# Optimization experiments

Measured on AMD Instinct MI355X. Metric: run time of the kernel, lower is better.

## Reference

```python
import jax, jax.numpy as jnp
from jax import lax
import numpy as np

NUM_KIND = 4
V, H, B = 34, 32, 4096   # raw vertical (2 rows dropped), horizontal, batch
KS = 33                  # odd-rounded max(V-2, H)
NUM_DEPTH = 4
N_SQ = 100


def _conv(x, w):
    # x: (N,1,h,w), w: (1,1,KS,KS); torch Conv2d == cross-correlation == lax default
    return lax.conv_general_dilated(x, w, (1, 1), 'SAME',
                                    dimension_numbers=('NCHW', 'OIHW', 'NCHW'))


def _conv_k(x, w):
    # x: (K,B,1,h,w) -> conv each map with the shared 1-channel kernel
    k, b, c, h, wd = x.shape
    return _conv(x.reshape(k * b, c, h, wd), w).reshape(k, b, c, h, wd)


def setup_inputs() -> dict:
    key = jax.random.key(0)
    ks = jax.random.split(key, 8)
    std = 0.3
    return {
        'dots':    jax.random.randint(ks[0], (V, H, B), 0, NUM_KIND + 1, dtype=jnp.int32),
        'w_each':  jax.random.normal(ks[1], (1, 1, KS, KS), jnp.float32) * std,
        'w_not':   jax.random.normal(ks[2], (1, 1, KS, KS), jnp.float32) * std,
        'w_not2':  jax.random.normal(ks[3], (1, 1, KS, KS), jnp.float32) * std,
        'w_empty': jax.random.normal(ks[4], (1, 1, KS, KS), jnp.float32) * std,
        'W1':      jax.random.normal(ks[5], (N_SQ, (V - 2) * H), jnp.float32) * std,
        'W2':      jax.random.normal(ks[6], (N_SQ, N_SQ), jnp.float32) * std,
        'W3':      jax.random.normal(ks[7], (1, N_SQ), jnp.float32) * std,
    }


def reference(dots, w_each, w_not, w_not2, w_empty, W1, W2, W3):
    # drop last 2 vertical rows, layout (V-2,H,B) -> (B,1,V-2,H)
    board = dots[:-2].astype(jnp.float32).transpose(2, 0, 1)[:, None]  # (B,1,h,w)

    empty = (board == 0).astype(jnp.float32)
    E = _conv(empty, w_empty)                                           # (B,1,h,w)

    kinds = jnp.arange(1, NUM_KIND + 1, dtype=board.dtype).reshape(NUM_KIND, 1, 1, 1, 1)
    each = (board[None] == kinds).astype(jnp.float32)                   # (K,B,1,h,w)
    notm = ((each + empty[None]) == 0).astype(jnp.float32)              # (K,B,1,h,w)

    # first pass: per-color value, masked to that color's cells
    notm_conv = _conv_k(notm, w_not)      # note: the torch code LOGS the convolved not-mask
    v = _conv_k(each, w_each) + E[None] - notm_conv
    L = each * v                          # each_color_value_log (masked)
    s = jax.nn.sigmoid(L.sum(axis=0))     # all_color_value_2nd, (B,1,h,w)

    # iterative diffusion; torch mutates the log in-place each depth:
    # L <- mask * (L + E + conv2nd(notm_conv * before)); before is detached
    for _ in range(NUM_DEPTH):
        before = lax.stop_gradient(s)
        C = _conv_k(notm_conv * before[None], w_not2)
        L = each * (L + E[None] + C)
        s = jax.nn.sigmoid(L.sum(axis=0))

    feat = s.reshape(s.shape[0], -1)      # (B, (V-2)*H)
    x = jax.nn.leaky_relu(feat @ W1.T, 0.2)
    x = jax.nn.leaky_relu(x @ W2.T, 0.2)
    return x @ W3.T                        # (B,1)
```

## Files before the change

### kernel.cpp

```cpp
#include <hip/hip_runtime.h>
#include <cstdint>
#include <cstddef>


typedef _Float16 f16;
typedef __attribute__((ext_vector_type(8))) _Float16 f16x8;
typedef __attribute__((ext_vector_type(4))) float f32x4;

#define NB   4096
#define PIX  1024
#define MR   (NB * 4)

__device__ __forceinline__ void gld_lds16(const void* g, void* l) {
    __builtin_amdgcn_global_load_lds(
        (const __attribute__((address_space(1))) void*)g,
        (__attribute__((address_space(3))) void*)l, 16, 0, 0);
}

__global__ void build_all(const float* __restrict__ we, const float* __restrict__ wn,
                          const float* __restrict__ wn2, const float* __restrict__ wem,
                          const float* __restrict__ W1, const int* __restrict__ dots,
                          f16* __restrict__ Me, f16* __restrict__ Mn,
                          f16* __restrict__ Mn2, f16* __restrict__ Mem,
                          f16* __restrict__ W1b, unsigned char* __restrict__ board) {
    __shared__ unsigned char tile[64][68];
    int bi = blockIdx.x, t = threadIdx.x;
    if (bi < 4096) {
        int idx = bi * 256 + t;
        int o = idx >> 10, in = idx & 1023;
        int i = o >> 5, j = o & 31, a = in >> 5, b = in & 31;
        int u = a - i + 16, v = b - j + 16;
        bool ok = (u >= 0) && (u < 33) && (v >= 0) && (v < 33);
        int w = u * 33 + v;
        float ve = 0.f, vn = 0.f, vn2 = 0.f, vem = 0.f;
        if (ok) { ve = we[w]; vn = wn[w]; vn2 = wn2[w]; vem = wem[w]; }
        Me[idx]  = (f16)ve;
        Mn[idx]  = (f16)vn;
        Mn2[idx] = (f16)vn2;
        Mem[idx] = (f16)vem;
    } else if (bi < 4608) {
        int idx = (bi - 4096) * 256 + t;
        int j = idx >> 10, i = idx & 1023;
        W1b[idx] = (f16)(j < 100 ? W1[j * 1024 + i] : 0.f);
    } else {
        int bb = bi - 4608;
        int bp = bb & 15, bn = bb >> 4;
        int p0 = bp * 64, n0 = bn * 64;
        int ln = t & 63, lp = t >> 6;
#pragma unroll
        for (int j = 0; j < 16; j++) {
            int p = lp * 16 + j;
            tile[p][ln] = (unsigned char)dots[(size_t)(p0 + p) * 4096 + n0 + ln];
        }
        __syncthreads();
#pragma unroll
        for (int j = 0; j < 16; j++) {
            int n = lp * 16 + j;
            board[(size_t)(n0 + n) * 1024 + p0 + ln] = tile[ln][n];
        }
    }
}

__global__ void expand_masks(const unsigned char* __restrict__ board,
                             f16* __restrict__ eachF, f16* __restrict__ notmF,
                             f16* __restrict__ emptyF) {
    int bi = blockIdx.x, t = threadIdx.x;
    if (bi < 8192) {
        int idx = bi * 256 + t;
        int r = idx >> 7, w0 = (idx & 127) << 3;
        int n = r >> 2, k1 = (r & 3) + 1;
        uint64_t bb = *(const uint64_t*)(board + (size_t)n * 1024 + w0);
        f16x8 e, m;
#pragma unroll
        for (int j = 0; j < 8; j++) {
            int bj = (int)((bb >> (8 * j)) & 0xff);
            e[j] = (bj == k1) ? (f16)1.f : (f16)0.f;
            m[j] = (bj != 0 && bj != k1) ? (f16)1.f : (f16)0.f;
        }
        *(f16x8*)(eachF + (size_t)idx * 8) = e;
        *(f16x8*)(notmF + (size_t)idx * 8) = m;
    } else {
        int idx = (bi - 8192) * 256 + t;
        int n = idx >> 7, w0 = (idx & 127) << 3;
        uint64_t bb = *(const uint64_t*)(board + (size_t)n * 1024 + w0);
        f16x8 e;
#pragma unroll
        for (int j = 0; j < 8; j++)
            e[j] = (((bb >> (8 * j)) & 0xff) == 0) ? (f16)1.f : (f16)0.f;
        *(f16x8*)(emptyF + (size_t)idx * 8) = e;
    }
}

template <int MODE>
__device__ __forceinline__ void run_gemm(
    int bjob, int ypx, int nx, char* smem,
    const f16* __restrict__ X, const f16* __restrict__ B,
    const unsigned char* __restrict__ board, const f16* __restrict__ En,
    const f16* __restrict__ NCs, f16* __restrict__ Lsel,
    f16* __restrict__ Sout, f16* __restrict__ outB, int ldo) {
    char* smB = smem;
    char* smA = smem + 16384;

    const int tid = threadIdx.x;
    const int wv = tid >> 6, ln = tid & 63;
    const int wm = wv >> 1, wn_ = wv & 1;
    const int lr = ln & 15, lq = ln >> 4;

    int xcd = bjob & 7, slot = bjob >> 3;
    int bx = slot % nx;
    int by = xcd * ypx + slot / nx;
    const int rtile = by * 128, otile = bx * 128;

    const f32x4 fz = {0.f, 0.f, 0.f, 0.f};
    f32x4 acc[4][4];
#pragma unroll
    for (int i = 0; i < 4; i++)
#pragma unroll
        for (int j = 0; j < 4; j++) acc[i][j] = fz;

    for (int kb = 0; kb < 1024; kb += 64) {
#pragma unroll
        for (int t = 0; t < 4; t++) {
            int c = (wv * 4 + t) * 64 + ln;
            int row = c >> 3, gcol = (c & 7) ^ (row & 7);
            gld_lds16(B + (size_t)(otile + row) * 1024 + kb + gcol * 8, smB + c * 16);
            gld_lds16(X + (size_t)(rtile + row) * 1024 + kb + gcol * 8, smA + c * 16);
        }
        __syncthreads();

#pragma unroll
        for (int kk = 0; kk < 2; kk++) {
            const int oct = kk * 4 + lq;
            f16x8 af[4], bfr[4];
#pragma unroll
            for (int i = 0; i < 4; i++) {
                int rrow = wm * 64 + i * 16 + lr;
                af[i] = *(const f16x8*)(smA + rrow * 128 + (oct ^ (rrow & 7)) * 16);
            }
#pragma unroll
            for (int j = 0; j < 4; j++) {
                int brow = wn_ * 64 + j * 16 + lr;
                bfr[j] = *(const f16x8*)(smB + brow * 128 + (oct ^ (brow & 7)) * 16);
            }
#pragma unroll
            for (int i = 0; i < 4; i++)
#pragma unroll
                for (int j = 0; j < 4; j++)
                    acc[i][j] = __builtin_amdgcn_mfma_f32_16x16x32_f16(
                        af[i], bfr[j], acc[i][j], 0, 0, 0);
        }
        __syncthreads();
    }

#pragma unroll
    for (int i = 0; i < 4; i++) {
        int rbase = rtile + wm * 64 + i * 16 + lq * 4;
#pragma unroll
        for (int j = 0; j < 4; j++) {
            int o = otile + wn_ * 64 + j * 16 + lr;
            f32x4 a = acc[i][j];
            if (MODE == 0) {
#pragma unroll
                for (int v = 0; v < 4; v++)
                    outB[(size_t)(rbase + v) * ldo + o] = (f16)a[v];
            } else {
                int n = rbase >> 2;
                size_t no = (size_t)n * PIX + o;
                int c = board[no];
                float L = 0.f;
                if (c > 0) {
                    float asel = (c == 1) ? a[0] : (c == 2) ? a[1]
                               : (c == 3) ? a[2] : a[3];
                    float ncsel = (float)NCs[(size_t)(rbase + c - 1) * PIX + o];
                    L = asel + (float)En[no] - ncsel;
                }
                Lsel[no] = (f16)L;
                Sout[no] = (f16)(1.f / (1.f + __expf(-L)));
            }
        }
    }
}

__global__ void __launch_bounds__(256, 4) gemm_faA(
    const f16* __restrict__ Mn, const f16* __restrict__ Mem,
    const f16* __restrict__ notmF, const f16* __restrict__ emptyF,
    f16* __restrict__ NC, f16* __restrict__ En) {
    __shared__ __attribute__((aligned(16))) char smem[32768];
    int bi = blockIdx.x;
    if (bi < 1024) {
        run_gemm<0>(bi, 16, 8, smem, notmF, Mn, nullptr, nullptr,
                    nullptr, nullptr, nullptr, NC, PIX);
    } else {
        run_gemm<0>(bi - 1024, 4, 8, smem, emptyF, Mem, nullptr, nullptr,
                    nullptr, nullptr, nullptr, En, PIX);
    }
}

__global__ void __launch_bounds__(256, 4) gemm_faB(
    const f16* __restrict__ Me, const f16* __restrict__ eachF,
    const unsigned char* __restrict__ board, const f16* __restrict__ En,
    const f16* __restrict__ NC, f16* __restrict__ Lsel, f16* __restrict__ S1) {
    __shared__ __attribute__((aligned(16))) char smem[32768];
    run_gemm<2>(blockIdx.x, 16, 8, smem, eachF, Me, board, En, NC,
                Lsel, S1, nullptr, 0);
}

__global__ void __launch_bounds__(256, 2) gemm_depth(
    const f16* __restrict__ NC, const f16* __restrict__ Mn2,
    const unsigned char* __restrict__ board, const f16* __restrict__ En,
    const f16* __restrict__ Sin, f16* __restrict__ Lsel,
    f16* __restrict__ Sout) {
    __shared__ __attribute__((aligned(16))) char smem[36864];
    char* smB = smem;
    char* smA = smem + 16384;
    char* smS = smem + 32768;

    const int tid = threadIdx.x;
    const int wv = tid >> 6, ln = tid & 63;
    const int wm = wv >> 1, wn_ = wv & 1;
    const int lr = ln & 15, lq = ln >> 4;

    int bi = blockIdx.x;
    int xcd = bi & 7, slot = bi >> 3;
    int bx = slot & 7;
    int by = xcd * 16 + (slot >> 3);
    const int rtile = by * 128, otile = bx * 128;
    const int n0 = rtile >> 2;

    const f32x4 fz = {0.f, 0.f, 0.f, 0.f};
    f32x4 acc[4][4];
#pragma unroll
    for (int i = 0; i < 4; i++)
#pragma unroll
        for (int j = 0; j < 4; j++) acc[i][j] = fz;

    for (int kb = 0; kb < 1024; kb += 64) {
#pragma unroll
        for (int t = 0; t < 4; t++) {
            int c = (wv * 4 + t) * 64 + ln;
            int row = c >> 3, gcol = (c & 7) ^ (row & 7);
            gld_lds16(Mn2 + (size_t)(otile + row) * 1024 + kb + gcol * 8, smB + c * 16);
            gld_lds16(NC  + (size_t)(rtile + row) * 1024 + kb + gcol * 8, smA + c * 16);
        }
        {
            int row = tid >> 3, col = tid & 7;
            gld_lds16(Sin + (size_t)(n0 + row) * 1024 + kb + col * 8, smS + tid * 16);
        }
        __syncthreads();

#pragma unroll
        for (int kk = 0; kk < 2; kk++) {
            const int oct = kk * 4 + lq;
            f16x8 af[4], bfr[4];
#pragma unroll
            for (int i = 0; i < 4; i++) {
                int rrow = wm * 64 + i * 16 + lr;
                f16x8 nv = *(const f16x8*)(smA + rrow * 128 + (oct ^ (rrow & 7)) * 16);
                f16x8 sv = *(const f16x8*)(smS + (rrow >> 2) * 128 + oct * 16);
                af[i] = nv * sv;
            }
#pragma unroll
            for (int j = 0; j < 4; j++) {
                int brow = wn_ * 64 + j * 16 + lr;
                bfr[j] = *(const f16x8*)(smB + brow * 128 + (oct ^ (brow & 7)) * 16);
            }
#pragma unroll
            for (int i = 0; i < 4; i++)
#pragma unroll
                for (int j = 0; j < 4; j++)
                    acc[i][j] = __builtin_amdgcn_mfma_f32_16x16x32_f16(
                        af[i], bfr[j], acc[i][j], 0, 0, 0);
        }
        __syncthreads();
    }

#pragma unroll
    for (int i = 0; i < 4; i++) {
        int rbase = rtile + wm * 64 + i * 16 + lq * 4;
#pragma unroll
        for (int j = 0; j < 4; j++) {
            int o = otile + wn_ * 64 + j * 16 + lr;
            f32x4 a = acc[i][j];
            int n = rbase >> 2;
            size_t no = (size_t)n * PIX + o;
            int c = board[no];
            float Lnew = 0.f;
            if (c > 0) {
                float asel = (c == 1) ? a[0] : (c == 2) ? a[1]
                           : (c == 3) ? a[2] : a[3];
                Lnew = (float)Lsel[no] + (float)En[no] + asel;
            }
            Lsel[no] = (f16)Lnew;
            Sout[no] = (f16)(1.f / (1.f + __expf(-Lnew)));
        }
    }
}

__global__ void __launch_bounds__(256) gemm_mlp_fused(
    const f16* __restrict__ feat, const f16* __restrict__ W1b,
    const float* __restrict__ W2, const float* __restrict__ W3,
    float* __restrict__ out) {
    __shared__ __attribute__((aligned(16))) char smem[47360];
    char* smB = smem;
    char* smA = smem + 16384;

    const int tid = threadIdx.x;
    const int wv = tid >> 6, ln = tid & 63;
    const int wm = wv >> 1, wn_ = wv & 1;
    const int lr = ln & 15, lq = ln >> 4;
    const int rtile = blockIdx.x * 128;

    const f32x4 fz = {0.f, 0.f, 0.f, 0.f};
    f32x4 acc[4][4];
#pragma unroll
    for (int i = 0; i < 4; i++)
#pragma unroll
        for (int j = 0; j < 4; j++) acc[i][j] = fz;

    for (int kb = 0; kb < 1024; kb += 64) {
#pragma unroll
        for (int t = 0; t < 4; t++) {
            int c = (wv * 4 + t) * 64 + ln;
            int row = c >> 3, gcol = (c & 7) ^ (row & 7);
            gld_lds16(W1b  + (size_t)row * 1024 + kb + gcol * 8, smB + c * 16);
            gld_lds16(feat + (size_t)(rtile + row) * 1024 + kb + gcol * 8, smA + c * 16);
        }
        __syncthreads();
#pragma unroll
        for (int kk = 0; kk < 2; kk++) {
            const int oct = kk * 4 + lq;
            f16x8 af[4], bfr[4];
#pragma unroll
            for (int i = 0; i < 4; i++) {
                int rrow = wm * 64 + i * 16 + lr;
                af[i] = *(const f16x8*)(smA + rrow * 128 + (oct ^ (rrow & 7)) * 16);
            }
#pragma unroll
            for (int j = 0; j < 4; j++) {
                int brow = wn_ * 64 + j * 16 + lr;
                bfr[j] = *(const f16x8*)(smB + brow * 128 + (oct ^ (brow & 7)) * 16);
            }
#pragma unroll
            for (int i = 0; i < 4; i++)
#pragma unroll
                for (int j = 0; j < 4; j++)
                    acc[i][j] = __builtin_amdgcn_mfma_f32_16x16x32_f16(
                        af[i], bfr[j], acc[i][j], 0, 0, 0);
        }
        __syncthreads();
    }

    float* xs  = (float*)smem;
    f16*   sW2 = (f16*)(smem + 25856);
    float* sW3 = (float*)(smem + 45856);
    float* red = (float*)(smem + 46272);
    for (int idx = tid; idx < 10000; idx += 256) sW2[idx] = (f16)W2[idx];
    if (tid < 100) sW3[tid] = W3[tid];

    for (int half = 0; half < 2; half++) {
        if (wm == half) {
#pragma unroll
            for (int i = 0; i < 4; i++) {
                int rb = i * 16 + lq * 4;
#pragma unroll
                for (int j = 0; j < 4; j++) {
                    int o = wn_ * 64 + j * 16 + lr;
                    if (o < 100) {
                        f32x4 a = acc[i][j];
#pragma unroll
                        for (int v = 0; v < 4; v++) {
                            float x = a[v];
                            xs[(rb + v) * 101 + o] = x > 0.f ? x : 0.2f * x;
                        }
                    }
                }
            }
        }
        __syncthreads();
        int nb = tid >> 2, q = tid & 3;
        const float* xrow = xs + nb * 101;
        float partial = 0.f;
        for (int jj = 0; jj < 25; jj++) {
            int j = q + jj * 4;
            const f16* w2r = sW2 + j * 100;
            float a2 = 0.f;
#pragma unroll
            for (int i = 0; i < 100; i++) a2 += (float)w2r[i] * xrow[i];
            partial += sW3[j] * (a2 > 0.f ? a2 : 0.2f * a2);
        }
        red[tid] = partial;
        __syncthreads();
        if (q == 0)
            out[rtile + half * 64 + nb] = red[tid] + red[tid + 1] + red[tid + 2] + red[tid + 3];
        __syncthreads();
    }
}

extern "C" void kernel_launch(void* const* d_in, const int* in_sizes, int n_in,
                              void* d_out, int out_size, void* d_ws, size_t ws_size,
                              hipStream_t stream) {
    (void)in_sizes; (void)n_in; (void)out_size; (void)ws_size;
    const int*   dots   = (const int*)d_in[0];
    const float* w_each = (const float*)d_in[1];
    const float* w_not  = (const float*)d_in[2];
    const float* w_not2 = (const float*)d_in[3];
    const float* w_emp  = (const float*)d_in[4];
    const float* W1 = (const float*)d_in[5];
    const float* W2 = (const float*)d_in[6];
    const float* W3 = (const float*)d_in[7];
    float* out = (float*)d_out;

    char* ws = (char*)d_ws;
    size_t off = 0;
    auto alloc = [&](size_t bytes) -> char* {
        char* p = ws + off;
        off += (bytes + 255) & ~(size_t)255;
        return p;
    };
    f16* Me    = (f16*)alloc((size_t)PIX * PIX * 2);
    f16* Mn    = (f16*)alloc((size_t)PIX * PIX * 2);
    f16* Mn2   = (f16*)alloc((size_t)PIX * PIX * 2);
    f16* Mem   = (f16*)alloc((size_t)PIX * PIX * 2);
    f16* W1b   = (f16*)alloc((size_t)128 * PIX * 2);
    unsigned char* board = (unsigned char*)alloc((size_t)NB * PIX);
    f16* eachF = (f16*)alloc((size_t)MR * PIX * 2);
    f16* notmF = (f16*)alloc((size_t)MR * PIX * 2);
    f16* emptyF= (f16*)alloc((size_t)NB * PIX * 2);
    f16* NC    = (f16*)alloc((size_t)MR * PIX * 2);
    f16* En    = (f16*)alloc((size_t)NB * PIX * 2);
    f16* Lsel  = (f16*)alloc((size_t)NB * PIX * 2);
    f16* Sa    = (f16*)alloc((size_t)NB * PIX * 2);
    f16* Sb    = (f16*)alloc((size_t)NB * PIX * 2);

    dim3 blk(256);
    build_all<<<5632, blk, 0, stream>>>(w_each, w_not, w_not2, w_emp, W1, dots,
                                        Me, Mn, Mn2, Mem, W1b, board);
    expand_masks<<<10240, blk, 0, stream>>>(board, eachF, notmF, emptyF);
    gemm_faA<<<1280, blk, 0, stream>>>(Mn, Mem, notmF, emptyF, NC, En);
    gemm_faB<<<1024, blk, 0, stream>>>(Me, eachF, board, En, NC, Lsel, Sa);
    gemm_depth<<<1024, blk, 0, stream>>>(NC, Mn2, board, En, Sa, Lsel, Sb);
    gemm_depth<<<1024, blk, 0, stream>>>(NC, Mn2, board, En, Sb, Lsel, Sa);
    gemm_depth<<<1024, blk, 0, stream>>>(NC, Mn2, board, En, Sa, Lsel, Sb);
    gemm_depth<<<1024, blk, 0, stream>>>(NC, Mn2, board, En, Sb, Lsel, Sa);
    gemm_mlp_fused<<<32, blk, 0, stream>>>(Sa, W1b, W2, W3, out);
}
```

Before: 446.9 us.

## Use 256x256 double-buffered 8-wave GEMM tiles and precompute NC*S operand in epilogue

Replaces the 128x128 single-buffered 4-wave GEMM with a 256x256, 512-thread kernel. It uses 128KB of LDS for double-buffered stages, interleaved quadrant MFMA scheduling with setprio and explicit waitcnt/barriers. The depth iterations no longer multiply NC by S while loading operands. Each epilogue instead writes the product NC*sigmoid into the reused notmF/eachF buffers, so the next GEMM reads a plain A matrix. This costs extra 4x-sized global writes per pass and gives lower occupancy, in exchange for more operand reuse and better load/compute overlap.

```diff
diff --git a/kernel.cpp b/kernel.cpp
--- a/kernel.cpp
+++ b/kernel.cpp
@@ -91,209 +91,210 @@
     }
 }
 
+#define READA(MH) \
+    _Pragma("unroll") for (int i = 0; i < 4; i++) \
+    _Pragma("unroll") for (int kk = 0; kk < 2; kk++) { \
+        int rr = wm * 64 + i * 16 + lr; \
+        aF[i][kk] = *(const f16x8*)(smem + bufo + (MH) * 16384 + rr * 128 + \
+                                    (((kk * 4 + lq) ^ (rr & 7)) * 16)); \
+    }
+
+#define READB(NH) \
+    _Pragma("unroll") for (int j = 0; j < 2; j++) \
+    _Pragma("unroll") for (int kk = 0; kk < 2; kk++) { \
+        int cc = wn * 32 + j * 16 + lr; \
+        bF[j][kk] = *(const f16x8*)(smem + bufo + 32768 + (NH) * 16384 + cc * 128 + \
+                                    (((kk * 4 + lq) ^ (cc & 7)) * 16)); \
+    }
+
+#define MFMAQ(MH, NH) \
+    _Pragma("unroll") for (int i = 0; i < 4; i++) \
+    _Pragma("unroll") for (int j = 0; j < 2; j++) \
+    _Pragma("unroll") for (int kk = 0; kk < 2; kk++) \
+        acc[MH][NH][i][j] = __builtin_amdgcn_mfma_f32_16x16x32_f16( \
+            aF[i][kk], bF[j][kk], acc[MH][NH][i][j], 0, 0, 0);
+
+#define STAGEA(TT, H) { \
+    int bo = ((TT) & 1) * 65536 + (H) * 16384; \
+    _Pragma("unroll") for (int s = 0; s < 2; s++) { \
+        int c = s * 512 + tid; int row = c >> 3; int gc = (c & 7) ^ (row & 7); \
+        gld_lds16(Ag + (size_t)(rtile + (H) * 128 + row) * 1024 + (TT) * 64 + gc * 8, \
+                  smem + bo + c * 16); } }
+
+#define STAGEB(TT, H) { \
+    int bo = ((TT) & 1) * 65536 + 32768 + (H) * 16384; \
+    _Pragma("unroll") for (int s = 0; s < 2; s++) { \
+        int c = s * 512 + tid; int row = c >> 3; int gc = (c & 7) ^ (row & 7); \
+        gld_lds16(Bg + (size_t)(otile + (H) * 128 + row) * 1024 + (TT) * 64 + gc * 8, \
+                  smem + bo + c * 16); } }
+
 template <int MODE>
-__device__ __forceinline__ void run_gemm(
-    int bjob, int ypx, int nx, char* smem,
-    const f16* __restrict__ X, const f16* __restrict__ B,
+__device__ __forceinline__ void gemm8_run(
+    int bjob, int nyt8, char* smem,
+    const f16* __restrict__ Ag, const f16* __restrict__ Bg,
     const unsigned char* __restrict__ board, const f16* __restrict__ En,
-    const f16* __restrict__ NCs, f16* __restrict__ Lsel,
-    f16* __restrict__ Sout, f16* __restrict__ outB, int ldo) {
-    char* smB = smem;
-    char* smA = smem + 16384;
-
+    const f16* __restrict__ NC, f16* __restrict__ Lsel,
+    f16* __restrict__ Pout, f16* __restrict__ outB, int ldo) {
     const int tid = threadIdx.x;
     const int wv = tid >> 6, ln = tid & 63;
-    const int wm = wv >> 1, wn_ = wv & 1;
+    const int wm = wv >> 2, wn = wv & 3;
     const int lr = ln & 15, lq = ln >> 4;
 
-    int xcd = bjob & 7, slot = bjob >> 3;
-    int bx = slot % nx;
-    int by = xcd * ypx + slot / nx;
-    const int rtile = by * 128, otile = bx * 128;
+    int xcd = bjob & 7, idx = bjob >> 3;
+    int bx = idx & 3;
+    int by = xcd * nyt8 + (idx >> 2);
+    const int rtile = by * 256, otile = bx * 256;
 
     const f32x4 fz = {0.f, 0.f, 0.f, 0.f};
-    f32x4 acc[4][4];
-#pragma unroll
-    for (int i = 0; i < 4; i++)
-#pragma unroll
-        for (int j = 0; j < 4; j++) acc[i][j] = fz;
-
-    for (int kb = 0; kb < 1024; kb += 64) {
-#pragma unroll
-        for (int t = 0; t < 4; t++) {
-            int c = (wv * 4 + t) * 64 + ln;
-            int row = c >> 3, gcol = (c & 7) ^ (row & 7);
-            gld_lds16(B + (size_t)(otile + row) * 1024 + kb + gcol * 8, smB + c * 16);
-            gld_lds16(X + (size_t)(rtile + row) * 1024 + kb + gcol * 8, smA + c * 16);
-        }
-        __syncthreads();
-
-#pragma unroll
-        for (int kk = 0; kk < 2; kk++) {
-            const int oct = kk * 4 + lq;
-            f16x8 af[4], bfr[4];
-#pragma unroll
-            for (int i = 0; i < 4; i++) {
-                int rrow = wm * 64 + i * 16 + lr;
-                af[i] = *(const f16x8*)(smA + rrow * 128 + (oct ^ (rrow & 7)) * 16);
-            }
-#pragma unroll
-            for (int j = 0; j < 4; j++) {
-                int brow = wn_ * 64 + j * 16 + lr;
-                bfr[j] = *(const f16x8*)(smB + brow * 128 + (oct ^ (brow & 7)) * 16);
-            }
+    f32x4 acc[2][2][4][2];
+#pragma unroll
+    for (int mh = 0; mh < 2; mh++)
+#pragma unroll
+        for (int nh = 0; nh < 2; nh++)
 #pragma unroll
             for (int i = 0; i < 4; i++)
 #pragma unroll
-                for (int j = 0; j < 4; j++)
-                    acc[i][j] = __builtin_amdgcn_mfma_f32_16x16x32_f16(
-                        af[i], bfr[j], acc[i][j], 0, 0, 0);
-        }
-        __syncthreads();
-    }
-
-#pragma unroll
-    for (int i = 0; i < 4; i++) {
-        int rbase = rtile + wm * 64 + i * 16 + lq * 4;
-#pragma unroll
-        for (int j = 0; j < 4; j++) {
-            int o = otile + wn_ * 64 + j * 16 + lr;
-            f32x4 a = acc[i][j];
-            if (MODE == 0) {
-#pragma unroll
-                for (int v = 0; v < 4; v++)
-                    outB[(size_t)(rbase + v) * ldo + o] = (f16)a[v];
-            } else {
-                int n = rbase >> 2;
-                size_t no = (size_t)n * PIX + o;
-                int c = board[no];
-                float L = 0.f;
-                if (c > 0) {
-                    float asel = (c == 1) ? a[0] : (c == 2) ? a[1]
-                               : (c == 3) ? a[2] : a[3];
-                    float ncsel = (float)NCs[(size_t)(rbase + c - 1) * PIX + o];
-                    L = asel + (float)En[no] - ncsel;
+                for (int j = 0; j < 2; j++) acc[mh][nh][i][j] = fz;
+
+    f16x8 aF[4][2], bF[2][2];
+
+    STAGEA(0, 0) STAGEB(0, 0) STAGEA(0, 1) STAGEB(0, 1)
+    STAGEB(1, 0) STAGEA(1, 1)
+    asm volatile("s_waitcnt vmcnt(4)" ::: "memory");
+    __builtin_amdgcn_s_barrier();
+
+    for (int t = 0; t < 16; t++) {
+        const int bufo = (t & 1) * 65536;
+        READA(0) READB(0)
+        if (t < 15) STAGEA(t + 1, 0)
+        __builtin_amdgcn_s_barrier();
+        asm volatile("s_waitcnt lgkmcnt(0)" ::: "memory");
+        __builtin_amdgcn_s_setprio(1);
+        MFMAQ(0, 0)
+        __builtin_amdgcn_s_setprio(0);
+        __builtin_amdgcn_s_barrier();
+        READA(1)
+        if (t < 15) STAGEB(t + 1, 1)
+        __builtin_amdgcn_s_barrier();
+        asm volatile("s_waitcnt lgkmcnt(0)" ::: "memory");
+        __builtin_amdgcn_s_setprio(1);
+        MFMAQ(1, 0)
+        __builtin_amdgcn_s_setprio(0);
+        __builtin_amdgcn_s_barrier();
+        READB(1)
+        if (t < 14) STAGEB(t + 2, 0)
+        __builtin_amdgcn_s_barrier();
+        asm volatile("s_waitcnt lgkmcnt(0)" ::: "memory");
+        __builtin_amdgcn_s_setprio(1);
+        MFMAQ(1, 1)
+        __builtin_amdgcn_s_setprio(0);
+        __builtin_amdgcn_s_barrier();
+        READA(0)
+        if (t < 14) STAGEA(t + 2, 1)
+        __builtin_amdgcn_s_barrier();
+        asm volatile("s_waitcnt lgkmcnt(0)" ::: "memory");
+        __builtin_amdgcn_s_setprio(1);
+        MFMAQ(0, 1)
+        __builtin_amdgcn_s_setprio(0);
+        if (t < 14) { asm volatile("s_waitcnt vmcnt(4)" ::: "memory"); }
+        else        { asm volatile("s_waitcnt vmcnt(0)" ::: "memory"); }
+        __builtin_amdgcn_s_barrier();
+    }
+
+#pragma unroll
+    for (int mh = 0; mh < 2; mh++)
+#pragma unroll
+        for (int nh = 0; nh < 2; nh++)
+#pragma unroll
+            for (int i = 0; i < 4; i++)
+#pragma unroll
+                for (int j = 0; j < 2; j++) {
+                    f32x4 a = acc[mh][nh][i][j];
+                    int rbase = rtile + mh * 128 + wm * 64 + i * 16 + lq * 4;
+                    int o = otile + nh * 128 + wn * 32 + j * 16 + lr;
+                    if constexpr (MODE == 0) {
+#pragma unroll
+                        for (int v = 0; v < 4; v++)
+                            outB[(size_t)(rbase + v) * ldo + o] = (f16)a[v];
+                    } else if constexpr (MODE == 2) {
+                        int n = rbase >> 2;
+                        size_t no = (size_t)n * PIX + o;
+                        int c = board[no];
+                        size_t r0 = (size_t)rbase * PIX + o;
+                        f16 nc0 = NC[r0], nc1 = NC[r0 + PIX];
+                        f16 nc2 = NC[r0 + 2 * PIX], nc3 = NC[r0 + 3 * PIX];
+                        float L = 0.f;
+                        if (c > 0) {
+                            float asel = (c == 1) ? a[0] : (c == 2) ? a[1]
+                                       : (c == 3) ? a[2] : a[3];
+                            float ncsel = (float)((c == 1) ? nc0 : (c == 2) ? nc1
+                                                : (c == 3) ? nc2 : nc3);
+                            L = asel + (float)En[no] - ncsel;
+                        }
+                        Lsel[no] = (f16)L;
+                        f16 s = (f16)(1.f / (1.f + __expf(-L)));
+                        Pout[r0]           = nc0 * s;
+                        Pout[r0 + PIX]     = nc1 * s;
+                        Pout[r0 + 2 * PIX] = nc2 * s;
+                        Pout[r0 + 3 * PIX] = nc3 * s;
+                    } else {
+                        int n = rbase >> 2;
+                        size_t no = (size_t)n * PIX + o;
+                        int c = board[no];
+                        float Lnew = 0.f;
+                        if (c > 0) {
+                            float asel = (c == 1) ? a[0] : (c == 2) ? a[1]
+                                       : (c == 3) ? a[2] : a[3];
+                            Lnew = (float)Lsel[no] + (float)En[no] + asel;
+                        }
+                        f16 s = (f16)(1.f / (1.f + __expf(-Lnew)));
+                        if constexpr (MODE == 4) {
+                            outB[no] = s;
+                        } else {
+                            Lsel[no] = (f16)Lnew;
+                            size_t r0 = (size_t)rbase * PIX + o;
+                            Pout[r0]           = NC[r0] * s;
+                            Pout[r0 + PIX]     = NC[r0 + PIX] * s;
+                            Pout[r0 + 2 * PIX] = NC[r0 + 2 * PIX] * s;
+                            Pout[r0 + 3 * PIX] = NC[r0 + 3 * PIX] * s;
+                        }
+                    }
                 }
-                Lsel[no] = (f16)L;
-                Sout[no] = (f16)(1.f / (1.f + __expf(-L)));
-            }
-        }
-    }
-}
-
-__global__ void __launch_bounds__(256, 4) gemm_faA(
+}
+
+__global__ void __launch_bounds__(512, 2) gemm8_faA(
     const f16* __restrict__ Mn, const f16* __restrict__ Mem,
     const f16* __restrict__ notmF, const f16* __restrict__ emptyF,
     f16* __restrict__ NC, f16* __restrict__ En) {
-    __shared__ __attribute__((aligned(16))) char smem[32768];
+    __shared__ __attribute__((aligned(16))) char smem[131072];
     int bi = blockIdx.x;
-    if (bi < 1024) {
-        run_gemm<0>(bi, 16, 8, smem, notmF, Mn, nullptr, nullptr,
-                    nullptr, nullptr, nullptr, NC, PIX);
+    if (bi < 256) {
+        gemm8_run<0>(bi, 8, smem, notmF, Mn, nullptr, nullptr, nullptr,
+                     nullptr, nullptr, NC, PIX);
     } else {
-        run_gemm<0>(bi - 1024, 4, 8, smem, emptyF, Mem, nullptr, nullptr,
-                    nullptr, nullptr, nullptr, En, PIX);
-    }
-}
-
-__global__ void __launch_bounds__(256, 4) gemm_faB(
+        gemm8_run<0>(bi - 256, 2, smem, emptyF, Mem, nullptr, nullptr, nullptr,
+                     nullptr, nullptr, En, PIX);
+    }
+}
+
+__global__ void __launch_bounds__(512, 2) gemm8_faB(
     const f16* __restrict__ Me, const f16* __restrict__ eachF,
     const unsigned char* __restrict__ board, const f16* __restrict__ En,
-    const f16* __restrict__ NC, f16* __restrict__ Lsel, f16* __restrict__ S1) {
-    __shared__ __attribute__((aligned(16))) char smem[32768];
-    run_gemm<2>(blockIdx.x, 16, 8, smem, eachF, Me, board, En, NC,
-                Lsel, S1, nullptr, 0);
-}
-
-__global__ void __launch_bounds__(256, 2) gemm_depth(
-    const f16* __restrict__ NC, const f16* __restrict__ Mn2,
+    const f16* __restrict__ NC, f16* __restrict__ Lsel, f16* __restrict__ P1) {
+    __shared__ __attribute__((aligned(16))) char smem[131072];
+    gemm8_run<2>(blockIdx.x, 8, smem, eachF, Me, board, En, NC, Lsel, P1,
+                 nullptr, 0);
+}
+
+template <int MODE>
+__global__ void __launch_bounds__(512, 2) gemm8_depth(
+    const f16* __restrict__ Pin, const f16* __restrict__ Mn2,
     const unsigned char* __restrict__ board, const f16* __restrict__ En,
-    const f16* __restrict__ Sin, f16* __restrict__ Lsel,
-    f16* __restrict__ Sout) {
-    __shared__ __attribute__((aligned(16))) char smem[36864];
-    char* smB = smem;
-    char* smA = smem + 16384;
-    char* smS = smem + 32768;
-
-    const int tid = threadIdx.x;
-    const int wv = tid >> 6, ln = tid & 63;
-    const int wm = wv >> 1, wn_ = wv & 1;
-    const int lr = ln & 15, lq = ln >> 4;
-
-    int bi = blockIdx.x;
-    int xcd = bi & 7, slot = bi >> 3;
-    int bx = slot & 7;
-    int by = xcd * 16 + (slot >> 3);
-    const int rtile = by * 128, otile = bx * 128;
-    const int n0 = rtile >> 2;
-
-    const f32x4 fz = {0.f, 0.f, 0.f, 0.f};
-    f32x4 acc[4][4];
-#pragma unroll
-    for (int i = 0; i < 4; i++)
-#pragma unroll
-        for (int j = 0; j < 4; j++) acc[i][j] = fz;
-
-    for (int kb = 0; kb < 1024; kb += 64) {
-#pragma unroll
-        for (int t = 0; t < 4; t++) {
-            int c = (wv * 4 + t) * 64 + ln;
-            int row = c >> 3, gcol = (c & 7) ^ (row & 7);
-            gld_lds16(Mn2 + (size_t)(otile + row) * 1024 + kb + gcol * 8, smB + c * 16);
-            gld_lds16(NC  + (size_t)(rtile + row) * 1024 + kb + gcol * 8, smA + c * 16);
-        }
-        {
-            int row = tid >> 3, col = tid & 7;
-            gld_lds16(Sin + (size_t)(n0 + row) * 1024 + kb + col * 8, smS + tid * 16);
-        }
-        __syncthreads();
-
-#pragma unroll
-        for (int kk = 0; kk < 2; kk++) {
-            const int oct = kk * 4 + lq;
-            f16x8 af[4], bfr[4];
-#pragma unroll
-            for (int i = 0; i < 4; i++) {
-                int rrow = wm * 64 + i * 16 + lr;
-                f16x8 nv = *(const f16x8*)(smA + rrow * 128 + (oct ^ (rrow & 7)) * 16);
-                f16x8 sv = *(const f16x8*)(smS + (rrow >> 2) * 128 + oct * 16);
-                af[i] = nv * sv;
-            }
-#pragma unroll
-            for (int j = 0; j < 4; j++) {
-                int brow = wn_ * 64 + j * 16 + lr;
-                bfr[j] = *(const f16x8*)(smB + brow * 128 + (oct ^ (brow & 7)) * 16);
-            }
-#pragma unroll
-            for (int i = 0; i < 4; i++)
-#pragma unroll
-                for (int j = 0; j < 4; j++)
-                    acc[i][j] = __builtin_amdgcn_mfma_f32_16x16x32_f16(
-                        af[i], bfr[j], acc[i][j], 0, 0, 0);
-        }
-        __syncthreads();
-    }
-
-#pragma unroll
-    for (int i = 0; i < 4; i++) {
-        int rbase = rtile + wm * 64 + i * 16 + lq * 4;
-#pragma unroll
-        for (int j = 0; j < 4; j++) {
-            int o = otile + wn_ * 64 + j * 16 + lr;
-            f32x4 a = acc[i][j];
-            int n = rbase >> 2;
-            size_t no = (size_t)n * PIX + o;
-            int c = board[no];
-            float Lnew = 0.f;
-            if (c > 0) {
-                float asel = (c == 1) ? a[0] : (c == 2) ? a[1]
-                           : (c == 3) ? a[2] : a[3];
-                Lnew = (float)Lsel[no] + (float)En[no] + asel;
-            }
-            Lsel[no] = (f16)Lnew;
-            Sout[no] = (f16)(1.f / (1.f + __expf(-Lnew)));
-        }
-    }
+    const f16* __restrict__ NC, f16* __restrict__ Lsel,
+    f16* __restrict__ Pout, f16* __restrict__ feat) {
+    __shared__ __attribute__((aligned(16))) char smem[131072];
+    gemm8_run<MODE>(blockIdx.x, 8, smem, Pin, Mn2, board, En, NC, Lsel, Pout,
+                    feat, 0);
 }
 
 __global__ void __launch_bounds__(256) gemm_mlp_fused(
@@ -429,18 +430,19 @@
     f16* NC    = (f16*)alloc((size_t)MR * PIX * 2);
     f16* En    = (f16*)alloc((size_t)NB * PIX * 2);
     f16* Lsel  = (f16*)alloc((size_t)NB * PIX * 2);
-    f16* Sa    = (f16*)alloc((size_t)NB * PIX * 2);
-    f16* Sb    = (f16*)alloc((size_t)NB * PIX * 2);
-
-    dim3 blk(256);
+    f16* feat  = (f16*)alloc((size_t)NB * PIX * 2);
+    f16* Pa = notmF;
+    f16* Pb = eachF;
+
+    dim3 blk(256), blk8(512);
     build_all<<<5632, blk, 0, stream>>>(w_each, w_not, w_not2, w_emp, W1, dots,
                                         Me, Mn, Mn2, Mem, W1b, board);
     expand_masks<<<10240, blk, 0, stream>>>(board, eachF, notmF, emptyF);
-    gemm_faA<<<1280, blk, 0, stream>>>(Mn, Mem, notmF, emptyF, NC, En);
-    gemm_faB<<<1024, blk, 0, stream>>>(Me, eachF, board, En, NC, Lsel, Sa);
-    gemm_depth<<<1024, blk, 0, stream>>>(NC, Mn2, board, En, Sa, Lsel, Sb);
-    gemm_depth<<<1024, blk, 0, stream>>>(NC, Mn2, board, En, Sb, Lsel, Sa);
-    gemm_depth<<<1024, blk, 0, stream>>>(NC, Mn2, board, En, Sa, Lsel, Sb);
-    gemm_depth<<<1024, blk, 0, stream>>>(NC, Mn2, board, En, Sb, Lsel, Sa);
-    gemm_mlp_fused<<<32, blk, 0, stream>>>(Sa, W1b, W2, W3, out);
-}
+    gemm8_faA<<<320, blk8, 0, stream>>>(Mn, Mem, notmF, emptyF, NC, En);
+    gemm8_faB<<<256, blk8, 0, stream>>>(Me, eachF, board, En, NC, Lsel, Pa);
+    gemm8_depth<3><<<256, blk8, 0, stream>>>(Pa, Mn2, board, En, NC, Lsel, Pb, nullptr);
+    gemm8_depth<3><<<256, blk8, 0, stream>>>(Pb, Mn2, board, En, NC, Lsel, Pa, nullptr);
+    gemm8_depth<3><<<256, blk8, 0, stream>>>(Pa, Mn2, board, En, NC, Lsel, Pb, nullptr);
+    gemm8_depth<4><<<256, blk8, 0, stream>>>(Pb, Mn2, board, En, NC, Lsel, nullptr, feat);
+    gemm_mlp_fused<<<32, blk, 0, stream>>>(feat, W1b, W2, W3, out);
+}
```

Result: slower. 472.3 us (+5.7%).

## Fuse first pass and all diffusion depths into one chained GEMM kernel

Applied to the files above, without the earlier changes.

Replaces the separate not-mask, first-pass and four depth GEMM launches with a single kernel. Each block owns a 64-row strip (16 boards) and walks all six passes itself. L values stay in registers, the sigmoid state stays in double-buffered LDS, and board colours are packed into registers, so the global Lsel and S round-trips and several launches go away. The inner loop adds double-buffered direct-to-LDS loads with explicit vmcnt waits and priority hints. In exchange, the full B matrix is re-streamed per 64-row strip, which raises weight traffic. The large LDS footprint limits residency to one 8-wave block per CU, and the En GEMM moves to its own small kernel.

```diff
diff --git a/kernel.cpp b/kernel.cpp
--- a/kernel.cpp
+++ b/kernel.cpp
@@ -91,13 +91,10 @@
     }
 }
 
-template <int MODE>
-__device__ __forceinline__ void run_gemm(
-    int bjob, int ypx, int nx, char* smem,
-    const f16* __restrict__ X, const f16* __restrict__ B,
-    const unsigned char* __restrict__ board, const f16* __restrict__ En,
-    const f16* __restrict__ NCs, f16* __restrict__ Lsel,
-    f16* __restrict__ Sout, f16* __restrict__ outB, int ldo) {
+__global__ void __launch_bounds__(256, 4) gemm_en(
+    const f16* __restrict__ Mem, const f16* __restrict__ emptyF,
+    f16* __restrict__ En) {
+    __shared__ __attribute__((aligned(16))) char smem[32768];
     char* smB = smem;
     char* smA = smem + 16384;
 
@@ -106,9 +103,10 @@
     const int wm = wv >> 1, wn_ = wv & 1;
     const int lr = ln & 15, lq = ln >> 4;
 
+    int bjob = blockIdx.x;
     int xcd = bjob & 7, slot = bjob >> 3;
-    int bx = slot % nx;
-    int by = xcd * ypx + slot / nx;
+    int bx = slot % 8;
+    int by = xcd * 4 + slot / 8;
     const int rtile = by * 128, otile = bx * 128;
 
     const f32x4 fz = {0.f, 0.f, 0.f, 0.f};
@@ -123,11 +121,10 @@
         for (int t = 0; t < 4; t++) {
             int c = (wv * 4 + t) * 64 + ln;
             int row = c >> 3, gcol = (c & 7) ^ (row & 7);
-            gld_lds16(B + (size_t)(otile + row) * 1024 + kb + gcol * 8, smB + c * 16);
-            gld_lds16(X + (size_t)(rtile + row) * 1024 + kb + gcol * 8, smA + c * 16);
-        }
-        __syncthreads();
-
+            gld_lds16(Mem    + (size_t)(otile + row) * 1024 + kb + gcol * 8, smB + c * 16);
+            gld_lds16(emptyF + (size_t)(rtile + row) * 1024 + kb + gcol * 8, smA + c * 16);
+        }
+        __syncthreads();
 #pragma unroll
         for (int kk = 0; kk < 2; kk++) {
             const int oct = kk * 4 + lq;
@@ -151,7 +148,6 @@
         }
         __syncthreads();
     }
-
 #pragma unroll
     for (int i = 0; i < 4; i++) {
         int rbase = rtile + wm * 64 + i * 16 + lq * 4;
@@ -159,140 +155,164 @@
         for (int j = 0; j < 4; j++) {
             int o = otile + wn_ * 64 + j * 16 + lr;
             f32x4 a = acc[i][j];
-            if (MODE == 0) {
-#pragma unroll
-                for (int v = 0; v < 4; v++)
-                    outB[(size_t)(rbase + v) * ldo + o] = (f16)a[v];
-            } else {
-                int n = rbase >> 2;
-                size_t no = (size_t)n * PIX + o;
-                int c = board[no];
-                float L = 0.f;
-                if (c > 0) {
-                    float asel = (c == 1) ? a[0] : (c == 2) ? a[1]
-                               : (c == 3) ? a[2] : a[3];
-                    float ncsel = (float)NCs[(size_t)(rbase + c - 1) * PIX + o];
-                    L = asel + (float)En[no] - ncsel;
-                }
-                Lsel[no] = (f16)L;
-                Sout[no] = (f16)(1.f / (1.f + __expf(-L)));
-            }
-        }
-    }
-}
-
-__global__ void __launch_bounds__(256, 4) gemm_faA(
-    const f16* __restrict__ Mn, const f16* __restrict__ Mem,
-    const f16* __restrict__ notmF, const f16* __restrict__ emptyF,
-    f16* __restrict__ NC, f16* __restrict__ En) {
-    __shared__ __attribute__((aligned(16))) char smem[32768];
-    int bi = blockIdx.x;
-    if (bi < 1024) {
-        run_gemm<0>(bi, 16, 8, smem, notmF, Mn, nullptr, nullptr,
-                    nullptr, nullptr, nullptr, NC, PIX);
-    } else {
-        run_gemm<0>(bi - 1024, 4, 8, smem, emptyF, Mem, nullptr, nullptr,
-                    nullptr, nullptr, nullptr, En, PIX);
-    }
-}
-
-__global__ void __launch_bounds__(256, 4) gemm_faB(
-    const f16* __restrict__ Me, const f16* __restrict__ eachF,
-    const unsigned char* __restrict__ board, const f16* __restrict__ En,
-    const f16* __restrict__ NC, f16* __restrict__ Lsel, f16* __restrict__ S1) {
-    __shared__ __attribute__((aligned(16))) char smem[32768];
-    run_gemm<2>(blockIdx.x, 16, 8, smem, eachF, Me, board, En, NC,
-                Lsel, S1, nullptr, 0);
-}
-
-__global__ void __launch_bounds__(256, 2) gemm_depth(
-    const f16* __restrict__ NC, const f16* __restrict__ Mn2,
-    const unsigned char* __restrict__ board, const f16* __restrict__ En,
-    const f16* __restrict__ Sin, f16* __restrict__ Lsel,
-    f16* __restrict__ Sout) {
-    __shared__ __attribute__((aligned(16))) char smem[36864];
+#pragma unroll
+            for (int v = 0; v < 4; v++)
+                En[(size_t)(rbase + v) * PIX + o] = (f16)a[v];
+        }
+    }
+}
+
+__global__ void __launch_bounds__(512, 2) fused_chain(
+    const f16* __restrict__ notmF, const f16* __restrict__ eachF,
+    const f16* __restrict__ Mn, const f16* __restrict__ Me,
+    const f16* __restrict__ Mn2, const unsigned char* __restrict__ board,
+    const f16* __restrict__ En, f16* __restrict__ NC, f16* __restrict__ feat) {
+    __shared__ __attribute__((aligned(16))) char smem[147968];
     char* smB = smem;
-    char* smA = smem + 16384;
-    char* smS = smem + 32768;
+    char* smA = smem + 65536;
+    f16* sBuf0 = (f16*)(smem + 81920);
+    f16* sBuf1 = (f16*)(smem + 81920 + 33024);
 
     const int tid = threadIdx.x;
     const int wv = tid >> 6, ln = tid & 63;
-    const int wm = wv >> 1, wn_ = wv & 1;
+    const int wm = wv >> 2, wn = wv & 3;
     const int lr = ln & 15, lq = ln >> 4;
 
     int bi = blockIdx.x;
-    int xcd = bi & 7, slot = bi >> 3;
-    int bx = slot & 7;
-    int by = xcd * 16 + (slot >> 3);
-    const int rtile = by * 128, otile = bx * 128;
+    const int by = (bi & 7) * 32 + (bi >> 3);
+    const int rtile = by * 64;
     const int n0 = rtile >> 2;
 
-    const f32x4 fz = {0.f, 0.f, 0.f, 0.f};
-    f32x4 acc[4][4];
-#pragma unroll
-    for (int i = 0; i < 4; i++)
-#pragma unroll
-        for (int j = 0; j < 4; j++) acc[i][j] = fz;
-
-    for (int kb = 0; kb < 1024; kb += 64) {
-#pragma unroll
-        for (int t = 0; t < 4; t++) {
-            int c = (wv * 4 + t) * 64 + ln;
-            int row = c >> 3, gcol = (c & 7) ^ (row & 7);
-            gld_lds16(Mn2 + (size_t)(otile + row) * 1024 + kb + gcol * 8, smB + c * 16);
-            gld_lds16(NC  + (size_t)(rtile + row) * 1024 + kb + gcol * 8, smA + c * 16);
-        }
-        {
-            int row = tid >> 3, col = tid & 7;
-            gld_lds16(Sin + (size_t)(n0 + row) * 1024 + kb + col * 8, smS + tid * 16);
-        }
-        __syncthreads();
-
-#pragma unroll
-        for (int kk = 0; kk < 2; kk++) {
-            const int oct = kk * 4 + lq;
-            f16x8 af[4], bfr[4];
-#pragma unroll
-            for (int i = 0; i < 4; i++) {
-                int rrow = wm * 64 + i * 16 + lr;
-                f16x8 nv = *(const f16x8*)(smA + rrow * 128 + (oct ^ (rrow & 7)) * 16);
-                f16x8 sv = *(const f16x8*)(smS + (rrow >> 2) * 128 + oct * 16);
-                af[i] = nv * sv;
-            }
-#pragma unroll
-            for (int j = 0; j < 4; j++) {
-                int brow = wn_ * 64 + j * 16 + lr;
-                bfr[j] = *(const f16x8*)(smB + brow * 128 + (oct ^ (brow & 7)) * 16);
-            }
-#pragma unroll
-            for (int i = 0; i < 4; i++)
-#pragma unroll
-                for (int j = 0; j < 4; j++)
-                    acc[i][j] = __builtin_amdgcn_mfma_f32_16x16x32_f16(
-                        af[i], bfr[j], acc[i][j], 0, 0, 0);
-        }
-        __syncthreads();
-    }
-
-#pragma unroll
-    for (int i = 0; i < 4; i++) {
-        int rbase = rtile + wm * 64 + i * 16 + lq * 4;
-#pragma unroll
-        for (int j = 0; j < 4; j++) {
-            int o = otile + wn_ * 64 + j * 16 + lr;
-            f32x4 a = acc[i][j];
-            int n = rbase >> 2;
-            size_t no = (size_t)n * PIX + o;
-            int c = board[no];
-            float Lnew = 0.f;
-            if (c > 0) {
-                float asel = (c == 1) ? a[0] : (c == 2) ? a[1]
-                           : (c == 3) ? a[2] : a[3];
-                Lnew = (float)Lsel[no] + (float)En[no] + asel;
-            }
-            Lsel[no] = (f16)Lnew;
-            Sout[no] = (f16)(1.f / (1.f + __expf(-Lnew)));
-        }
+    float Lr[4][2][4];
+    unsigned cpk[4] = {0u, 0u, 0u, 0u};
+
+    for (int p = 0; p < 6; p++) {
+        const f16* Asrc = (p == 0) ? notmF : (p == 1) ? eachF : NC;
+        const f16* Bsrc = (p == 0) ? Mn : (p == 1) ? Me : Mn2;
+        f16* sRd = (p & 1) ? sBuf1 : sBuf0;
+        f16* sWr = (p & 1) ? sBuf0 : sBuf1;
+
+#pragma unroll
+        for (int oc = 0; oc < 4; oc++) {
+            const int otile = oc * 256;
+            const f32x4 fz = {0.f, 0.f, 0.f, 0.f};
+            f32x4 acc[2][4];
+#pragma unroll
+            for (int i = 0; i < 2; i++)
+#pragma unroll
+                for (int j = 0; j < 4; j++) acc[i][j] = fz;
+
+            {
+#pragma unroll
+                for (int s2 = 0; s2 < 4; s2++) {
+                    int c = s2 * 512 + tid;
+                    int row = c >> 3, gc = (c & 7) ^ (row & 7);
+                    gld_lds16(Bsrc + (size_t)(otile + row) * 1024 + gc * 8,
+                              smB + c * 16);
+                }
+                int row = tid >> 3, gc = (tid & 7) ^ (row & 7);
+                gld_lds16(Asrc + (size_t)(rtile + row) * 1024 + gc * 8,
+                          smA + tid * 16);
+            }
+
+            for (int t = 0; t < 16; t++) {
+                if (t < 15) {
+                    int bn = (t + 1) & 1;
+#pragma unroll
+                    for (int s2 = 0; s2 < 4; s2++) {
+                        int c = s2 * 512 + tid;
+                        int row = c >> 3, gc = (c & 7) ^ (row & 7);
+                        gld_lds16(Bsrc + (size_t)(otile + row) * 1024 + (t + 1) * 64 + gc * 8,
+                                  smB + bn * 32768 + c * 16);
+                    }
+                    int row = tid >> 3, gc = (tid & 7) ^ (row & 7);
+                    gld_lds16(Asrc + (size_t)(rtile + row) * 1024 + (t + 1) * 64 + gc * 8,
+                              smA + bn * 8192 + tid * 16);
+                    asm volatile("s_waitcnt vmcnt(5)" ::: "memory");
+                } else {
+                    asm volatile("s_waitcnt vmcnt(0)" ::: "memory");
+                }
+                __builtin_amdgcn_s_barrier();
+
+                const int bo = t & 1;
+#pragma unroll
+                for (int kk = 0; kk < 2; kk++) {
+                    const int oct = kk * 4 + lq;
+                    f16x8 af[2], bf[4];
+#pragma unroll
+                    for (int i = 0; i < 2; i++) {
+                        int rr = wm * 32 + i * 16 + lr;
+                        f16x8 v = *(const f16x8*)(smA + bo * 8192 + rr * 128 +
+                                                  ((oct ^ (rr & 7)) * 16));
+                        if (p >= 2) {
+                            const f16* sp = sRd + (rr >> 2) * 1032 + t * 64 + oct * 8;
+                            v = v * *(const f16x8*)sp;
+                        }
+                        af[i] = v;
+                    }
+#pragma unroll
+                    for (int j = 0; j < 4; j++) {
+                        int cc = wn * 64 + j * 16 + lr;
+                        bf[j] = *(const f16x8*)(smB + bo * 32768 + cc * 128 +
+                                                ((oct ^ (cc & 7)) * 16));
+                    }
+                    __builtin_amdgcn_s_setprio(1);
+#pragma unroll
+                    for (int i = 0; i < 2; i++)
+#pragma unroll
+                        for (int j = 0; j < 4; j++)
+                            acc[i][j] = __builtin_amdgcn_mfma_f32_16x16x32_f16(
+                                af[i], bf[j], acc[i][j], 0, 0, 0);
+                    __builtin_amdgcn_s_setprio(0);
+                }
+                __builtin_amdgcn_s_barrier();
+            }
+
+#pragma unroll
+            for (int i = 0; i < 2; i++) {
+                const int rb = wm * 32 + i * 16 + lq * 4;
+                const int nl = rb >> 2;
+#pragma unroll
+                for (int j = 0; j < 4; j++) {
+                    const int o = otile + wn * 64 + j * 16 + lr;
+                    const size_t no = (size_t)(n0 + nl) * PIX + o;
+                    const int q = i * 4 + j;
+                    f32x4 a = acc[i][j];
+                    if (p == 0) {
+#pragma unroll
+                        for (int v = 0; v < 4; v++)
+                            NC[(size_t)(rtile + rb + v) * PIX + o] = (f16)a[v];
+                        unsigned c = board[no];
+                        cpk[oc] |= c << (q * 4);
+                    } else {
+                        int c = (cpk[oc] >> (q * 4)) & 15;
+                        float L = 0.f;
+                        if (c > 0) {
+                            float asel = (c == 1) ? a[0] : (c == 2) ? a[1]
+                                       : (c == 3) ? a[2] : a[3];
+                            float E = (float)En[no];
+                            if (p == 1) {
+                                float ncsel = (float)NC[(size_t)(rtile + rb + c - 1) * PIX + o];
+                                L = asel + E - ncsel;
+                            } else {
+                                L = Lr[oc][i][j] + E + asel;
+                            }
+                        }
+                        Lr[oc][i][j] = L;
+                        float s = 1.f / (1.f + __expf(-L));
+                        sWr[nl * 1032 + o] = (f16)s;
+                    }
+                }
+            }
+            __syncthreads();
+        }
+        __syncthreads();
+    }
+
+    for (int idx = tid; idx < 2048; idx += 512) {
+        int nl = idx >> 7, o8 = (idx & 127) << 3;
+        f16x8 v = *(const f16x8*)(sBuf0 + nl * 1032 + o8);
+        *(f16x8*)(feat + (size_t)(n0 + nl) * PIX + o8) = v;
     }
 }
 
@@ -428,19 +448,14 @@
     f16* emptyF= (f16*)alloc((size_t)NB * PIX * 2);
     f16* NC    = (f16*)alloc((size_t)MR * PIX * 2);
     f16* En    = (f16*)alloc((size_t)NB * PIX * 2);
-    f16* Lsel  = (f16*)alloc((size_t)NB * PIX * 2);
-    f16* Sa    = (f16*)alloc((size_t)NB * PIX * 2);
-    f16* Sb    = (f16*)alloc((size_t)NB * PIX * 2);
-
-    dim3 blk(256);
+    f16* feat  = (f16*)alloc((size_t)NB * PIX * 2);
+
+    dim3 blk(256), blkF(512);
     build_all<<<5632, blk, 0, stream>>>(w_each, w_not, w_not2, w_emp, W1, dots,
                                         Me, Mn, Mn2, Mem, W1b, board);
     expand_masks<<<10240, blk, 0, stream>>>(board, eachF, notmF, emptyF);
-    gemm_faA<<<1280, blk, 0, stream>>>(Mn, Mem, notmF, emptyF, NC, En);
-    gemm_faB<<<1024, blk, 0, stream>>>(Me, eachF, board, En, NC, Lsel, Sa);
-    gemm_depth<<<1024, blk, 0, stream>>>(NC, Mn2, board, En, Sa, Lsel, Sb);
-    gemm_depth<<<1024, blk, 0, stream>>>(NC, Mn2, board, En, Sb, Lsel, Sa);
-    gemm_depth<<<1024, blk, 0, stream>>>(NC, Mn2, board, En, Sa, Lsel, Sb);
-    gemm_depth<<<1024, blk, 0, stream>>>(NC, Mn2, board, En, Sb, Lsel, Sa);
-    gemm_mlp_fused<<<32, blk, 0, stream>>>(Sa, W1b, W2, W3, out);
-}
+    gemm_en<<<256, blk, 0, stream>>>(Mem, emptyF, En);
+    fused_chain<<<256, blkF, 0, stream>>>(notmF, eachF, Mn, Me, Mn2, board,
+                                          En, NC, feat);
+    gemm_mlp_fused<<<32, blk, 0, stream>>>(feat, W1b, W2, W3, out);
+}
```

New measurement: 501.3 us. +12.2%, slower.
